# Optimization experiments

Hardware: AMD Instinct MI355X
Metric: run time of the kernel (lower is better)

Reference implementation:

```python
import jax, jax.numpy as jnp
import numpy as np

N_GROUPS = 32
EPS = 1e-5
N_HEADS = 4
D_K = 64


def group_norm(x, gamma, beta):
    # x: [B, C, H, W]; normalize over (channels within group, spatial)
    B, C, H, W = x.shape
    xg = x.reshape(B, N_GROUPS, C // N_GROUPS, H, W)
    mean = jnp.mean(xg, axis=(2, 3, 4), keepdims=True)
    var = jnp.var(xg, axis=(2, 3, 4), keepdims=True)
    xn = ((xg - mean) * jax.lax.rsqrt(var + EPS)).reshape(B, C, H, W)
    return xn * gamma[None, :, None, None] + beta[None, :, None, None]


def setup_inputs() -> dict:
    key = jax.random.key(0)
    ks = jax.random.split(key, 4)
    B, C, H, W = 4, 256, 64, 64
    x = jax.random.normal(ks[0], (B, C, H, W), dtype=jnp.float32)
    gamma = jnp.ones((C,), dtype=jnp.float32)
    beta = jnp.zeros((C,), dtype=jnp.float32)
    w_qkv = jax.random.normal(ks[1], (C, N_HEADS * D_K * 3), dtype=jnp.float32) * (C ** -0.5)
    b_qkv = jnp.zeros((N_HEADS * D_K * 3,), dtype=jnp.float32)
    w_out = jax.random.normal(ks[2], (N_HEADS * D_K, C), dtype=jnp.float32) * ((N_HEADS * D_K) ** -0.5)
    b_out = jnp.zeros((C,), dtype=jnp.float32)
    return {"x": x, "gamma": gamma, "beta": beta, "w_qkv": w_qkv,
            "b_qkv": b_qkv, "w_out": w_out, "b_out": b_out}


def reference(x, gamma, beta, w_qkv, b_qkv, w_out, b_out):
    B, C, H, W = x.shape
    S = H * W
    scale = D_K ** -0.5
    # GroupNorm -> [B, S, C]
    h = group_norm(x, gamma, beta).reshape(B, C, S).transpose(0, 2, 1)
    qkv = (h @ w_qkv + b_qkv).reshape(B, S, N_HEADS, 3 * D_K)
    q, k, v = jnp.split(qkv, 3, axis=-1)          # each [B, S, H, D]
    attn = jnp.einsum('bihd,bjhd->bijh', q, k) * scale
    attn = jax.nn.softmax(attn, axis=2)           # softmax over j (keys)
    res = jnp.einsum('bijh,bjhd->bihd', attn, v)  # [B, S, H, D]
    res = res.reshape(B, S, N_HEADS * D_K)
    res = res @ w_out + b_out                     # [B, S, C]
    res = res.transpose(0, 2, 1).reshape(B, C, H, W)
    return res + x
```

## Files before the change

### kernel.cpp

```cpp
#include <hip/hip_runtime.h>
#include <hip/hip_bf16.h>


typedef __attribute__((ext_vector_type(8))) short short8;
typedef __attribute__((ext_vector_type(4))) float f32x4;
typedef __attribute__((ext_vector_type(16))) float f32x16;

__device__ __forceinline__ unsigned short f2bf(float f) {
    union { float f; unsigned u; } v; v.f = f;
    unsigned r = v.u + 0x7FFF + ((v.u >> 16) & 1);
    return (unsigned short)(r >> 16);
}

__device__ __forceinline__ unsigned cvt_pk_bf16(float lo, float hi) {
    unsigned r;
    asm("v_cvt_pk_bf16_f32 %0, %1, %2" : "=v"(r) : "v"(lo), "v"(hi));
    return r;
}

__device__ __forceinline__ void permswap(unsigned &x, unsigned &y) {
    asm("v_permlane32_swap_b32 %0, %1" : "+v"(x), "+v"(y));
}

__device__ __forceinline__ float fexp2(float x) {
    float r;
    asm("v_exp_f32 %0, %1" : "=v"(r) : "v"(x));
    return r;
}

__device__ __forceinline__ void gl_lds16(const void* g, void* l) {
    __builtin_amdgcn_global_load_lds(
        (const __attribute__((address_space(1))) void*)(g),
        (__attribute__((address_space(3))) void*)(l), 16, 0, 0);
}

__device__ __forceinline__ f32x16 fzero16() {
    f32x16 z;
    #pragma unroll
    for (int i = 0; i < 16; ++i) z[i] = 0.f;
    return z;
}

__global__ __launch_bounds__(1024) void k_gn_stats(const float* __restrict__ x,
                                                   float* __restrict__ stats) {
    int bg = blockIdx.x;
    const float4* xp = (const float4*)(x + bg * 32768);
    float s1 = 0.f, s2 = 0.f;
    for (int i = threadIdx.x; i < 8192; i += 1024) {
        float4 v = xp[i];
        s1 += v.x + v.y + v.z + v.w;
        s2 += v.x*v.x + v.y*v.y + v.z*v.z + v.w*v.w;
    }
    #pragma unroll
    for (int off = 32; off; off >>= 1) {
        s1 += __shfl_down(s1, off);
        s2 += __shfl_down(s2, off);
    }
    __shared__ float r1[16], r2[16];
    int wid = threadIdx.x >> 6;
    if ((threadIdx.x & 63) == 0) { r1[wid] = s1; r2[wid] = s2; }
    __syncthreads();
    if (threadIdx.x == 0) {
        float a = 0.f, b = 0.f;
        #pragma unroll
        for (int i = 0; i < 16; ++i) { a += r1[i]; b += r2[i]; }
        float mean = a * (1.f/32768.f);
        float var  = b * (1.f/32768.f) - mean*mean;
        stats[bg*2]   = mean;
        stats[bg*2+1] = rsqrtf(var + 1e-5f);
    }
}

__global__ void k_cvt_w(const float* __restrict__ wqkv, const float* __restrict__ wout,
                        unsigned short* __restrict__ wqkvT, unsigned short* __restrict__ woutT) {
    int i = blockIdx.x * 256 + threadIdx.x;
    if (i < 196608) {
        int k = i / 768, n = i - k * 768;
        wqkvT[n*256 + k] = f2bf(wqkv[i]);
    }
    if (i < 65536) {
        int k = i >> 8, n = i & 255;
        woutT[n*256 + k] = f2bf(wout[i]);
    }
}

__global__ __launch_bounds__(256) void k_gn_norm(
    const float* __restrict__ x, const float* __restrict__ gamma,
    const float* __restrict__ beta, const float* __restrict__ stats,
    unsigned short* __restrict__ h) {
    __shared__ unsigned short t[64][72];
    int s0 = blockIdx.x * 64, c0 = blockIdx.y * 64, b = blockIdx.z;
    int tid = threadIdx.x;
    int sl = (tid & 15) * 4;
    int cr = tid >> 4;
    #pragma unroll
    for (int p = 0; p < 4; ++p) {
        int c = c0 + cr + p * 16;
        float4 v = *(const float4*)&x[(b*256 + c)*4096 + s0 + sl];
        int sg = (b*32 + (c >> 3)) * 2;
        float mean = stats[sg], rstd = stats[sg+1];
        float sa = rstd * gamma[c];
        float sb = beta[c] - mean * sa;
        ushort4 pk;
        pk.x = f2bf(v.x*sa + sb); pk.y = f2bf(v.y*sa + sb);
        pk.z = f2bf(v.z*sa + sb); pk.w = f2bf(v.w*sa + sb);
        *(ushort4*)&t[cr + p*16][sl] = pk;
    }
    __syncthreads();
    int sr = tid >> 2;
    int cc = (tid & 3) * 16;
    unsigned rr[8];
    #pragma unroll
    for (int j = 0; j < 8; ++j)
        rr[j] = (unsigned)t[cc + 2*j][sr] | ((unsigned)t[cc + 2*j + 1][sr] << 16);
    unsigned short* hp = &h[(b*4096 + s0 + sr)*256 + c0];
    *(uint4*)&hp[cc]     = make_uint4(rr[0], rr[1], rr[2], rr[3]);
    *(uint4*)&hp[cc + 8] = make_uint4(rr[4], rr[5], rr[6], rr[7]);
}

__global__ __launch_bounds__(256) void k_qkv(
    const unsigned short* __restrict__ h, const unsigned short* __restrict__ wT,
    const float* __restrict__ bqkv,
    unsigned short* __restrict__ q, unsigned short* __restrict__ kk,
    unsigned short* __restrict__ vT) {
    int mt = blockIdx.x, head = blockIdx.y;
    int tid = threadIdx.x;
    int wid = tid >> 6, lane = tid & 63;
    int g = lane >> 4, li = lane & 15;
    int m0 = mt * 64 + wid * 16;
    int row = m0 + li;
    f32x4 acc[12];
    #pragma unroll
    for (int nt = 0; nt < 12; ++nt) acc[nt] = (f32x4){0.f,0.f,0.f,0.f};
    #pragma unroll
    for (int kt = 0; kt < 8; ++kt) {
        short8 a = *(const short8*)&h[row*256 + kt*32 + g*8];
        #pragma unroll
        for (int nt = 0; nt < 12; ++nt) {
            int n = head*192 + nt*16 + li;
            short8 b = *(const short8*)&wT[n*256 + kt*32 + g*8];
            acc[nt] = __builtin_amdgcn_mfma_f32_16x16x32_bf16(a, b, acc[nt], 0, 0, 0);
        }
    }
    int b = m0 >> 12;
    int s0 = m0 & 4095;
    int bh = b*4 + head;
    #pragma unroll
    for (int nt = 0; nt < 12; ++nt) {
        int ng = head*192 + nt*16 + li;
        float bias = bqkv[ng];
        int d = (nt & 3)*16 + li;
        if ((nt >> 2) == 2) {
            ushort4 pk;
            pk.x = f2bf(acc[nt][0] + bias); pk.y = f2bf(acc[nt][1] + bias);
            pk.z = f2bf(acc[nt][2] + bias); pk.w = f2bf(acc[nt][3] + bias);
            *(ushort4*)&vT[(bh*64 + d)*4096 + s0 + g*4] = pk;
        } else if ((nt >> 2) == 0) {
            #pragma unroll
            for (int r = 0; r < 4; ++r)
                q[(bh*4096 + s0 + g*4 + r)*64 + d] = f2bf((acc[nt][r] + bias) * 0.1803368801f);
        } else {
            #pragma unroll
            for (int r = 0; r < 4; ++r)
                kk[(bh*4096 + s0 + g*4 + r)*64 + d] = f2bf(acc[nt][r] + bias);
        }
    }
}

__global__ __launch_bounds__(512, 4) void k_attn(
    const unsigned short* __restrict__ q, const unsigned short* __restrict__ kk,
    const unsigned short* __restrict__ vT, unsigned short* __restrict__ ao) {
    __shared__ __align__(16) char smem[65536];

    int qt = blockIdx.x, bh = blockIdx.y;
    int tid = threadIdx.x;
    int wid = tid >> 6, lane = tid & 63;
    int qw = wid & 3, st = wid >> 2;
    int hi = lane >> 5, il = lane & 31;
    int swl = (il & 7) << 4;

    int qbase = qt * 128 + qw * 32;
    int qrow = bh * 4096 + qbase + il;
    short8 bq[4];
    #pragma unroll
    for (int kc = 0; kc < 4; ++kc)
        bq[kc] = *(const short8*)&q[qrow*64 + kc*16 + hi*8];

    unsigned p16  = tid * 16;
    unsigned row0 = p16 >> 7;
    unsigned sw   = (row0 & 7) << 4;
    unsigned ks0  = p16 ^ sw;
    unsigned vc0  = (p16 & 127u) ^ sw;
    const char* kbase = (const char*)kk + (size_t)bh * 524288;
    const char* vbase = (const char*)vT + (size_t)(bh*64 + row0) * 8192;
    unsigned woff = wid * 1024;

#define STAGE_PAIR(d, pair) do {                                             \
    const char* _k0 = kbase + (size_t)(2*(pair)) * 8192;                     \
    size_t _vo = (size_t)(2*(pair)) * 128;                                   \
    gl_lds16(_k0 + ks0,              smem + ((d)*2+0)*8192 + woff);          \
    gl_lds16(_k0 + 8192 + ks0,       smem + ((d)*2+1)*8192 + woff);          \
    gl_lds16(vbase + _vo + vc0,       smem + 32768 + ((d)*2+0)*8192 + woff); \
    gl_lds16(vbase + _vo + 128 + vc0, smem + 32768 + ((d)*2+1)*8192 + woff); \
} while (0)

    f32x16 o0 = fzero16(), o1 = fzero16();
    float m_run = -1e30f, l_loc = 0.f;

    STAGE_PAIR(0, 0);
    int cur = 0;
    for (int tp = 0; tp < 32; ++tp) {
        if (tp < 31) {
            STAGE_PAIR(cur ^ 1, tp + 1);
            asm volatile("s_waitcnt vmcnt(4)" ::: "memory");
        } else {
            asm volatile("s_waitcnt vmcnt(0)" ::: "memory");
        }
        __builtin_amdgcn_s_barrier();
        asm volatile("" ::: "memory");

        const char* kb = smem + (cur*2 + st) * 8192;
        const char* vb = smem + 32768 + (cur*2 + st) * 8192;

        f32x16 s0 = fzero16(), s1 = fzero16();
        __builtin_amdgcn_s_setprio(1);
        #pragma unroll
        for (int kc = 0; kc < 4; ++kc) {
            int c = (kc*32 + hi*16) ^ swl;
            short8 ka0 = *(const short8*)(kb + il*128 + c);
            short8 ka1 = *(const short8*)(kb + 4096 + il*128 + c);
            s0 = __builtin_amdgcn_mfma_f32_32x32x16_bf16(ka0, bq[kc], s0, 0, 0, 0);
            s1 = __builtin_amdgcn_mfma_f32_32x32x16_bf16(ka1, bq[kc], s1, 0, 0, 0);
        }
        __builtin_amdgcn_s_setprio(0);

        float mx = fmaxf(s0[0], s1[0]);
        #pragma unroll
        for (int r = 1; r < 16; ++r) mx = fmaxf(mx, fmaxf(s0[r], s1[r]));
        mx = fmaxf(mx, __shfl_xor(mx, 32));
        if (__any(mx > m_run)) {
            float m_new = fmaxf(m_run, mx);
            float fac = fexp2(m_run - m_new);
            l_loc *= fac;
            #pragma unroll
            for (int r = 0; r < 16; ++r) { o0[r] *= fac; o1[r] *= fac; }
            m_run = m_new;
        }
        float p0[16], p1[16];
        #pragma unroll
        for (int r = 0; r < 16; ++r) {
            p0[r] = fexp2(s0[r] - m_run);
            p1[r] = fexp2(s1[r] - m_run);
            l_loc += p0[r] + p1[r];
        }

        unsigned w[16];
        #pragma unroll
        for (int t = 0; t < 2; ++t) {
            const float* pp = t ? p1 : p0;
            #pragma unroll
            for (int hh = 0; hh < 2; ++hh) {
                unsigned a = cvt_pk_bf16(pp[hh*8+0], pp[hh*8+1]);
                unsigned b = cvt_pk_bf16(pp[hh*8+2], pp[hh*8+3]);
                unsigned c = cvt_pk_bf16(pp[hh*8+4], pp[hh*8+5]);
                unsigned d = cvt_pk_bf16(pp[hh*8+6], pp[hh*8+7]);
                permswap(a, c);
                permswap(b, d);
                int base = (t*2 + hh) * 4;
                w[base+0] = a; w[base+1] = b; w[base+2] = c; w[base+3] = d;
            }
        }

        __builtin_amdgcn_s_setprio(1);
        #pragma unroll
        for (int jc = 0; jc < 4; ++jc) {
            union { unsigned u[4]; short8 s8; } pb;
            pb.u[0] = w[jc*4+0]; pb.u[1] = w[jc*4+1];
            pb.u[2] = w[jc*4+2]; pb.u[3] = w[jc*4+3];
            int c = (jc*32 + hi*16) ^ swl;
            short8 va0 = *(const short8*)(vb + il*128 + c);
            short8 va1 = *(const short8*)(vb + 4096 + il*128 + c);
            o0 = __builtin_amdgcn_mfma_f32_32x32x16_bf16(va0, pb.s8, o0, 0, 0, 0);
            o1 = __builtin_amdgcn_mfma_f32_32x32x16_bf16(va1, pb.s8, o1, 0, 0, 0);
        }
        __builtin_amdgcn_s_setprio(0);

        asm volatile("" ::: "memory");
        __builtin_amdgcn_s_barrier();
        cur ^= 1;
    }
#undef STAGE_PAIR

    l_loc += __shfl_xor(l_loc, 32);

    float* red = (float*)smem;
    int slot = ((qw*64 + lane) * 34);
    if (st == 1) {
        #pragma unroll
        for (int r = 0; r < 16; ++r) { red[slot + r] = o0[r]; red[slot + 16 + r] = o1[r]; }
        red[slot + 32] = l_loc;
        red[slot + 33] = m_run;
    }
    __syncthreads();
    if (st == 0) {
        float m1 = red[slot + 33], l1 = red[slot + 32];
        float m = fmaxf(m_run, m1);
        float f0 = fexp2(m_run - m), f1 = fexp2(m1 - m);
        float inv = 1.f / (l_loc * f0 + l1 * f1);
        float a0 = f0 * inv, a1 = f1 * inv;
        int b = bh >> 2, hh = bh & 3;
        int s = qbase + il;
        unsigned short* aop = &ao[((size_t)(b*4096 + s))*256 + hh*64];
        #pragma unroll
        for (int rr = 0; rr < 4; ++rr) {
            ushort4 pk0, pk1;
            pk0.x = f2bf(o0[rr*4+0]*a0 + red[slot + rr*4+0]*a1);
            pk0.y = f2bf(o0[rr*4+1]*a0 + red[slot + rr*4+1]*a1);
            pk0.z = f2bf(o0[rr*4+2]*a0 + red[slot + rr*4+2]*a1);
            pk0.w = f2bf(o0[rr*4+3]*a0 + red[slot + rr*4+3]*a1);
            *(ushort4*)&aop[rr*8 + hi*4] = pk0;
            pk1.x = f2bf(o1[rr*4+0]*a0 + red[slot + 16 + rr*4+0]*a1);
            pk1.y = f2bf(o1[rr*4+1]*a0 + red[slot + 16 + rr*4+1]*a1);
            pk1.z = f2bf(o1[rr*4+2]*a0 + red[slot + 16 + rr*4+2]*a1);
            pk1.w = f2bf(o1[rr*4+3]*a0 + red[slot + 16 + rr*4+3]*a1);
            *(ushort4*)&aop[32 + rr*8 + hi*4] = pk1;
        }
    }
}

__global__ __launch_bounds__(256) void k_out(
    const unsigned short* __restrict__ ao, const unsigned short* __restrict__ wT,
    const float* __restrict__ bout, const float* __restrict__ x,
    float* __restrict__ out) {
    int mt = blockIdx.x, ntb = blockIdx.y;
    int tid = threadIdx.x;
    int wid = tid >> 6, lane = tid & 63;
    int g = lane >> 4, li = lane & 15;
    int m0 = mt * 64 + wid * 16;
    int row = m0 + li;
    f32x4 acc[4];
    #pragma unroll
    for (int nt = 0; nt < 4; ++nt) acc[nt] = (f32x4){0.f,0.f,0.f,0.f};
    #pragma unroll
    for (int kt = 0; kt < 8; ++kt) {
        short8 a = *(const short8*)&ao[row*256 + kt*32 + g*8];
        #pragma unroll
        for (int nt = 0; nt < 4; ++nt) {
            int n = ntb*64 + nt*16 + li;
            short8 b = *(const short8*)&wT[n*256 + kt*32 + g*8];
            acc[nt] = __builtin_amdgcn_mfma_f32_16x16x32_bf16(a, b, acc[nt], 0, 0, 0);
        }
    }
    int b = m0 >> 12;
    int s0 = (m0 & 4095) + g*4;
    #pragma unroll
    for (int nt = 0; nt < 4; ++nt) {
        int c = ntb*64 + nt*16 + li;
        float bias = bout[c];
        int base = (b*256 + c)*4096 + s0;
        float4 xr = *(const float4*)&x[base];
        float4 ov;
        ov.x = acc[nt][0] + bias + xr.x;
        ov.y = acc[nt][1] + bias + xr.y;
        ov.z = acc[nt][2] + bias + xr.z;
        ov.w = acc[nt][3] + bias + xr.w;
        *(float4*)&out[base] = ov;
    }
}

extern "C" void kernel_launch(void* const* d_in, const int* in_sizes, int n_in,
                              void* d_out, int out_size, void* d_ws, size_t ws_size,
                              hipStream_t stream) {
    (void)in_sizes; (void)n_in; (void)out_size; (void)ws_size;
    const float* x     = (const float*)d_in[0];
    const float* gamma = (const float*)d_in[1];
    const float* beta  = (const float*)d_in[2];
    const float* wqkv  = (const float*)d_in[3];
    const float* bqkv  = (const float*)d_in[4];
    const float* wout  = (const float*)d_in[5];
    const float* bout  = (const float*)d_in[6];
    float* out = (float*)d_out;

    char* ws = (char*)d_ws;
    unsigned short* h     = (unsigned short*)(ws);
    unsigned short* q     = (unsigned short*)(ws + (8u<<20));
    unsigned short* kk    = (unsigned short*)(ws + (16u<<20));
    unsigned short* vT    = (unsigned short*)(ws + (24u<<20));
    unsigned short* ao    = (unsigned short*)(ws + (32u<<20));
    unsigned short* wqkvT = (unsigned short*)(ws + (40u<<20));
    unsigned short* woutT = (unsigned short*)(ws + (40u<<20) + 393216);
    float*          stats = (float*)(ws + (40u<<20) + 524288);

    k_gn_stats<<<128, 1024, 0, stream>>>(x, stats);
    k_cvt_w<<<768, 256, 0, stream>>>(wqkv, wout, wqkvT, woutT);
    k_gn_norm<<<dim3(64, 4, 4), 256, 0, stream>>>(x, gamma, beta, stats, h);
    k_qkv<<<dim3(256, 4), 256, 0, stream>>>(h, wqkvT, bqkv, q, kk, vT);
    k_attn<<<dim3(32, 16), 512, 0, stream>>>(q, kk, vT, ao);
    k_out<<<dim3(256, 4), 256, 0, stream>>>(ao, woutT, bout, x, out);
}
```

Before: 187.2 us.

## Remap attention blocks, move load wait after PV, tree reductions, retile output GEMM

```diff
diff --git a/kernel.cpp b/kernel.cpp
--- a/kernel.cpp
+++ b/kernel.cpp
@@ -172,7 +172,9 @@
     const unsigned short* __restrict__ vT, unsigned short* __restrict__ ao) {
     __shared__ __align__(16) char smem[65536];
 
-    int qt = blockIdx.x, bh = blockIdx.y;
+    int n = blockIdx.x;
+    int qt = n >> 4;
+    int bh = ((n & 7) << 1) | ((n >> 3) & 1);
     int tid = threadIdx.x;
     int wid = tid >> 6, lane = tid & 63;
     int qw = wid & 3, st = wid >> 2;
@@ -208,16 +210,13 @@
     float m_run = -1e30f, l_loc = 0.f;
 
     STAGE_PAIR(0, 0);
+    asm volatile("s_waitcnt vmcnt(0)" ::: "memory");
+    __builtin_amdgcn_s_barrier();
+    asm volatile("" ::: "memory");
+
     int cur = 0;
     for (int tp = 0; tp < 32; ++tp) {
-        if (tp < 31) {
-            STAGE_PAIR(cur ^ 1, tp + 1);
-            asm volatile("s_waitcnt vmcnt(4)" ::: "memory");
-        } else {
-            asm volatile("s_waitcnt vmcnt(0)" ::: "memory");
-        }
-        __builtin_amdgcn_s_barrier();
-        asm volatile("" ::: "memory");
+        if (tp < 31) STAGE_PAIR(cur ^ 1, tp + 1);
 
         const char* kb = smem + (cur*2 + st) * 8192;
         const char* vb = smem + 32768 + (cur*2 + st) * 8192;
@@ -234,9 +233,12 @@
         }
         __builtin_amdgcn_s_setprio(0);
 
-        float mx = fmaxf(s0[0], s1[0]);
-        #pragma unroll
-        for (int r = 1; r < 16; ++r) mx = fmaxf(mx, fmaxf(s0[r], s1[r]));
+        float m8[8];
+        #pragma unroll
+        for (int r = 0; r < 8; ++r)
+            m8[r] = fmaxf(fmaxf(s0[2*r], s0[2*r+1]), fmaxf(s1[2*r], s1[2*r+1]));
+        float mx = fmaxf(fmaxf(fmaxf(m8[0], m8[1]), fmaxf(m8[2], m8[3])),
+                         fmaxf(fmaxf(m8[4], m8[5]), fmaxf(m8[6], m8[7])));
         mx = fmaxf(mx, __shfl_xor(mx, 32));
         if (__any(mx > m_run)) {
             float m_new = fmaxf(m_run, mx);
@@ -251,8 +253,13 @@
         for (int r = 0; r < 16; ++r) {
             p0[r] = fexp2(s0[r] - m_run);
             p1[r] = fexp2(s1[r] - m_run);
-            l_loc += p0[r] + p1[r];
-        }
+        }
+        float a8[8];
+        #pragma unroll
+        for (int r = 0; r < 8; ++r)
+            a8[r] = (p0[2*r] + p0[2*r+1]) + (p1[2*r] + p1[2*r+1]);
+        float ps = ((a8[0] + a8[1]) + (a8[2] + a8[3])) + ((a8[4] + a8[5]) + (a8[6] + a8[7]));
+        l_loc += ps;
 
         unsigned w[16];
         #pragma unroll
@@ -285,8 +292,10 @@
         }
         __builtin_amdgcn_s_setprio(0);
 
+        if (tp < 31) asm volatile("s_waitcnt vmcnt(0)" ::: "memory");
         asm volatile("" ::: "memory");
         __builtin_amdgcn_s_barrier();
+        asm volatile("" ::: "memory");
         cur ^= 1;
     }
 #undef STAGE_PAIR
@@ -332,30 +341,31 @@
     const unsigned short* __restrict__ ao, const unsigned short* __restrict__ wT,
     const float* __restrict__ bout, const float* __restrict__ x,
     float* __restrict__ out) {
-    int mt = blockIdx.x, ntb = blockIdx.y;
+    int mt = blockIdx.x;
     int tid = threadIdx.x;
     int wid = tid >> 6, lane = tid & 63;
     int g = lane >> 4, li = lane & 15;
-    int m0 = mt * 64 + wid * 16;
+    int rg = wid & 1, ch = wid >> 1;
+    int m0 = mt * 32 + rg * 16;
     int row = m0 + li;
-    f32x4 acc[4];
-    #pragma unroll
-    for (int nt = 0; nt < 4; ++nt) acc[nt] = (f32x4){0.f,0.f,0.f,0.f};
+    f32x4 acc[8];
+    #pragma unroll
+    for (int nt = 0; nt < 8; ++nt) acc[nt] = (f32x4){0.f,0.f,0.f,0.f};
     #pragma unroll
     for (int kt = 0; kt < 8; ++kt) {
         short8 a = *(const short8*)&ao[row*256 + kt*32 + g*8];
         #pragma unroll
-        for (int nt = 0; nt < 4; ++nt) {
-            int n = ntb*64 + nt*16 + li;
-            short8 b = *(const short8*)&wT[n*256 + kt*32 + g*8];
+        for (int nt = 0; nt < 8; ++nt) {
+            int nn = ch*128 + nt*16 + li;
+            short8 b = *(const short8*)&wT[nn*256 + kt*32 + g*8];
             acc[nt] = __builtin_amdgcn_mfma_f32_16x16x32_bf16(a, b, acc[nt], 0, 0, 0);
         }
     }
     int b = m0 >> 12;
     int s0 = (m0 & 4095) + g*4;
     #pragma unroll
-    for (int nt = 0; nt < 4; ++nt) {
-        int c = ntb*64 + nt*16 + li;
+    for (int nt = 0; nt < 8; ++nt) {
+        int c = ch*128 + nt*16 + li;
         float bias = bout[c];
         int base = (b*256 + c)*4096 + s0;
         float4 xr = *(const float4*)&x[base];
@@ -395,6 +405,6 @@
     k_cvt_w<<<768, 256, 0, stream>>>(wqkv, wout, wqkvT, woutT);
     k_gn_norm<<<dim3(64, 4, 4), 256, 0, stream>>>(x, gamma, beta, stats, h);
     k_qkv<<<dim3(256, 4), 256, 0, stream>>>(h, wqkvT, bqkv, q, kk, vT);
-    k_attn<<<dim3(32, 16), 512, 0, stream>>>(q, kk, vT, ao);
-    k_out<<<dim3(256, 4), 256, 0, stream>>>(ao, woutT, bout, x, out);
-}
+    k_attn<<<dim3(512), 512, 0, stream>>>(q, kk, vT, ao);
+    k_out<<<dim3(512), 256, 0, stream>>>(ao, woutT, bout, x, out);
+}
```

Result: faster. 180.5 us (-3.6%).
